# Kernel optimization log

Hardware: AMD Instinct MI355X
Metric: run time of the kernel (lower is better)

Reference implementation:

```python
import jax, jax.numpy as jnp
import numpy as np

B, L, K, D = 8, 4096, 16, 128


def setup_inputs() -> dict:
    key = jax.random.key(0)
    k1, k2 = jax.random.split(key)
    frame = jax.random.normal(k1, (B, L, 4, 3), dtype=jnp.float32)  # [B,L,4,3]: row0=center, rows1-3=frame axes
    attr = jax.random.normal(k2, (B, L, D), dtype=jnp.float32)
    return {"frame": frame, "attr": attr}


def reference(frame, attr):
    Kmax = 16
    center = frame[:, :, 0]  # [B,L,3]
    # pairwise squared distances (no grad needed through topk selection)
    c_ng = jax.lax.stop_gradient(center)
    diff = c_ng[:, :, None, :] - c_ng[:, None, :, :]  # [B,L,L,3]
    distance_sq = jnp.sum(diff * diff, axis=-1)  # [B,L,L]
    # k nearest neighbors (smallest distance)
    _, nbr = jax.lax.top_k(-distance_sq, Kmax)  # [B,L,K] int32 indices
    # gather neighbor attributes: attr[b, nbr[b,l,k], :]
    gathered_attr = jax.vmap(lambda a, i: a[i])(attr, nbr)  # [B,L,K,D]
    # gather neighbor centers and project delta into local frame
    nbr_center = jax.vmap(lambda c, i: c[i])(center, nbr)  # [B,L,K,3]
    delta = nbr_center - center[:, :, None, :]  # [B,L,K,3]
    euclidian = jnp.einsum('blkc,blcr->blkr', delta, frame[:, :, 1:4])  # [B,L,K,3]
    return (euclidian, gathered_attr)
```

## Files before the change

kernel.cpp:

```cpp
#include <hip/hip_runtime.h>
#include <stdint.h>

typedef unsigned long long u64;
typedef float nfloat4 __attribute__((ext_vector_type(4)));

#define LQ   4096
#define BQ   8
#define KNB  16
#define LPQ  8
#define TPB  256
#define QPB  (TPB / LPQ)
#define BPB  (LQ / QPB)

__device__ __forceinline__ double dmin(double a, double b) { return __builtin_fmin(a, b); }
__device__ __forceinline__ double dmax(double a, double b) { return __builtin_fmax(a, b); }


__global__ __launch_bounds__(TPB) void knn_fused_kernel(
    const float4* __restrict__ frame4,
    const float4* __restrict__ attr4,
    float* __restrict__ out_e,
    nfloat4* __restrict__ outg4)
{
    __shared__ float4 cpos[LQ];
    __shared__ int nbrs[QPB * KNB];

    const int b    = blockIdx.x >> 7;
    const int qblk = blockIdx.x & (BPB - 1);
    const int tid  = threadIdx.x;

    const float4* fb = frame4 + (size_t)b * LQ * 3;
    for (int j = tid; j < LQ; j += TPB) cpos[j] = fb[j * 3];
    __syncthreads();

    const int qloc = tid >> 3;
    const int h    = tid & 7;
    const int l    = qblk * QPB + qloc;
    const float4 me = cpos[l];

    double R[KNB];
#pragma unroll
    for (int i = 0; i < KNB; ++i) R[i] = 1.0;

#pragma unroll 1
    for (int bb = 0; bb < 32; ++bb) {
        double S[KNB];
#pragma unroll
        for (int t = 0; t < 16; ++t) {
            const int j = bb * 128 + t * 8 + h;
            const float4 p = cpos[j];
            const float dx = __fsub_rn(me.x, p.x);
            const float dy = __fsub_rn(me.y, p.y);
            const float dz = __fsub_rn(me.z, p.z);
            const float d  = __fadd_rn(__fadd_rn(__fmul_rn(dx, dx), __fmul_rn(dy, dy)),
                                       __fmul_rn(dz, dz));
            const u64 key = ((u64)__float_as_uint(d) << 12) | (unsigned)j;
            S[t] = __builtin_bit_cast(double, key);
        }
#pragma unroll
        for (int k = 2; k <= 16; k <<= 1) {
#pragma unroll
            for (int g = k >> 1; g >= 1; g >>= 1) {
#pragma unroll
                for (int i = 0; i < 16; ++i) {
                    if ((i & g) == 0) {
                        const int j2 = i + g;
                        const bool up = ((i & k) == 0);
                        const double lo = dmin(S[i], S[j2]);
                        const double hi = dmax(S[i], S[j2]);
                        S[i]  = up ? lo : hi;
                        S[j2] = up ? hi : lo;
                    }
                }
            }
        }
        double M[KNB];
#pragma unroll
        for (int i = 0; i < 16; ++i) M[i] = dmin(R[i], S[15 - i]);
#pragma unroll
        for (int g = 8; g >= 1; g >>= 1) {
#pragma unroll
            for (int i = 0; i < 16; ++i) {
                if ((i & g) == 0) {
                    const double lo = dmin(M[i], M[i + g]);
                    const double hi = dmax(M[i], M[i + g]);
                    M[i]     = lo;
                    M[i + g] = hi;
                }
            }
        }
#pragma unroll
        for (int i = 0; i < 16; ++i) R[i] = M[i];
    }

#pragma unroll
    for (int m = 1; m <= 4; m <<= 1) {
        double P[KNB];
#pragma unroll
        for (int i = 0; i < 16; ++i) P[i] = __shfl_xor(R[i], m, 64);
        double M[KNB];
#pragma unroll
        for (int i = 0; i < 16; ++i) M[i] = dmin(R[i], P[15 - i]);
#pragma unroll
        for (int g = 8; g >= 1; g >>= 1) {
#pragma unroll
            for (int i = 0; i < 16; ++i) {
                if ((i & g) == 0) {
                    const double lo = dmin(M[i], M[i + g]);
                    const double hi = dmax(M[i], M[i + g]);
                    M[i]     = lo;
                    M[i + g] = hi;
                }
            }
        }
#pragma unroll
        for (int i = 0; i < 16; ++i) R[i] = M[i];
    }

    if (h == 0) {
        const size_t gq = (size_t)b * LQ + l;
        const float4 f1 = fb[l * 3 + 1];
        const float4 f2 = fb[l * 3 + 2];
        const float R00 = me.w, R01 = f1.x, R02 = f1.y;
        const float R10 = f1.z, R11 = f1.w, R12 = f2.x;
        const float R20 = f2.y, R21 = f2.z, R22 = f2.w;

        float ebuf[48];
#pragma unroll
        for (int k = 0; k < KNB; ++k) {
            const u64 bits = __builtin_bit_cast(u64, R[k]);
            const int j = (int)(bits & 0xFFFu);
            nbrs[qloc * KNB + k] = j;
            const float4 p = cpos[j];
            const float dx = p.x - me.x;
            const float dy = p.y - me.y;
            const float dz = p.z - me.z;
            ebuf[k * 3 + 0] = dx * R00 + dy * R10 + dz * R20;
            ebuf[k * 3 + 1] = dx * R01 + dy * R11 + dz * R21;
            ebuf[k * 3 + 2] = dx * R02 + dy * R12 + dz * R22;
        }
        float4* eo = (float4*)(out_e + gq * 48);
#pragma unroll
        for (int t = 0; t < 12; ++t) eo[t] = ((const float4*)ebuf)[t];
    }

    __syncthreads();
    const float4* ab = attr4 + (((size_t)b) << 12) * 32;
    const size_t obase = ((size_t)b * LQ + (size_t)qblk * QPB) * (KNB * 32);
#pragma unroll 8
    for (int it = 0; it < 64; ++it) {
        const int fl   = it * TPB + tid;
        const int d4   = fl & 31;
        const int pair = fl >> 5;
        const int nb   = nbrs[pair];
        const float4 t4 = ab[(size_t)nb * 32 + d4];
        nfloat4 v = {t4.x, t4.y, t4.z, t4.w};
        __builtin_nontemporal_store(v, &outg4[obase + fl]);
    }
}

extern "C" void kernel_launch(void* const* d_in, const int* in_sizes, int n_in,
                              void* d_out, int out_size, void* d_ws, size_t ws_size,
                              hipStream_t stream)
{
    const float* frame = (const float*)d_in[0];
    const float* attr  = (const float*)d_in[1];
    float* out = (float*)d_out;

    nfloat4* outg4 = (nfloat4*)(out + (size_t)BQ * LQ * KNB * 3);
    knn_fused_kernel<<<BQ * BPB, TPB, 0, stream>>>(
        (const float4*)frame, (const float4*)attr, out, outg4);
}
```

Baseline: 363.5 us.

## Use truncated 32-bit keys for KNN filtering with exact double-key refinement

The candidate scan now packs a truncated distance (low 12 mantissa bits replaced by the index) into a 32-bit key. It runs an 8-element sort network plus a bitonic merge with integer compare-exchange instead of 64-bit fmin/fmax. The 32 best candidates per query are then re-ranked across lanes with exact 64-bit keys, so the final choice still matches the reference ordering. Positions move to SoA shared arrays, and the euclidean output is spread over four lanes. The attribute gather is re-indexed per wave so the block-wide barrier can be dropped. The risk is that heavy ties in the truncated keys could push a true neighbor out of the 32 survivors.

```diff
diff --git a/kernel.cpp b/kernel.cpp
--- a/kernel.cpp
+++ b/kernel.cpp
@@ -7,13 +7,28 @@
 #define LQ   4096
 #define BQ   8
 #define KNB  16
-#define LPQ  8
 #define TPB  256
-#define QPB  (TPB / LPQ)
+#define QPB  32
 #define BPB  (LQ / QPB)
 
-__device__ __forceinline__ double dmin(double a, double b) { return __builtin_fmin(a, b); }
-__device__ __forceinline__ double dmax(double a, double b) { return __builtin_fmax(a, b); }
+__device__ __forceinline__ void ceu(uint32_t &a, uint32_t &b) {
+    const uint32_t mn = a < b ? a : b;
+    const uint32_t mx = a < b ? b : a;
+    a = mn; b = mx;
+}
+__device__ __forceinline__ void ced(double &a, double &b) {
+    const double mn = __builtin_fmin(a, b);
+    const double mx = __builtin_fmax(a, b);
+    a = mn; b = mx;
+}
+__device__ __forceinline__ float dist2(float mx, float my, float mz,
+                                       float px, float py, float pz) {
+    const float dx = __fsub_rn(mx, px);
+    const float dy = __fsub_rn(my, py);
+    const float dz = __fsub_rn(mz, pz);
+    return __fadd_rn(__fadd_rn(__fmul_rn(dx, dx), __fmul_rn(dy, dy)),
+                     __fmul_rn(dz, dz));
+}
 
 
 __global__ __launch_bounds__(TPB) void knn_fused_kernel(
@@ -22,140 +37,247 @@
     float* __restrict__ out_e,
     nfloat4* __restrict__ outg4)
 {
-    __shared__ float4 cpos[LQ];
-    __shared__ int nbrs[QPB * KNB];
+    __shared__ float xs[LQ], ys[LQ], zs[LQ];
+    __shared__ unsigned short surv[QPB][32];
+    __shared__ int nbrs[QPB][KNB];
 
     const int b    = blockIdx.x >> 7;
     const int qblk = blockIdx.x & (BPB - 1);
     const int tid  = threadIdx.x;
 
     const float4* fb = frame4 + (size_t)b * LQ * 3;
-    for (int j = tid; j < LQ; j += TPB) cpos[j] = fb[j * 3];
+    for (int j = tid; j < LQ; j += TPB) {
+        const float4 v = fb[j * 3];
+        xs[j] = v.x; ys[j] = v.y; zs[j] = v.z;
+    }
     __syncthreads();
 
     const int qloc = tid >> 3;
     const int h    = tid & 7;
     const int l    = qblk * QPB + qloc;
-    const float4 me = cpos[l];
-
-    double R[KNB];
-#pragma unroll
-    for (int i = 0; i < KNB; ++i) R[i] = 1.0;
+    const float mx = xs[l], my = ys[l], mz = zs[l];
+
+    uint32_t R[16];
+#pragma unroll
+    for (int i = 0; i < 16; ++i) R[i] = 0xFFFFFFFFu;
 
 #pragma unroll 1
-    for (int bb = 0; bb < 32; ++bb) {
-        double S[KNB];
-#pragma unroll
-        for (int t = 0; t < 16; ++t) {
-            const int j = bb * 128 + t * 8 + h;
-            const float4 p = cpos[j];
-            const float dx = __fsub_rn(me.x, p.x);
-            const float dy = __fsub_rn(me.y, p.y);
-            const float dz = __fsub_rn(me.z, p.z);
-            const float d  = __fadd_rn(__fadd_rn(__fmul_rn(dx, dx), __fmul_rn(dy, dy)),
-                                       __fmul_rn(dz, dz));
-            const u64 key = ((u64)__float_as_uint(d) << 12) | (unsigned)j;
-            S[t] = __builtin_bit_cast(double, key);
-        }
-#pragma unroll
-        for (int k = 2; k <= 16; k <<= 1) {
-#pragma unroll
-            for (int g = k >> 1; g >= 1; g >>= 1) {
-#pragma unroll
-                for (int i = 0; i < 16; ++i) {
-                    if ((i & g) == 0) {
-                        const int j2 = i + g;
-                        const bool up = ((i & k) == 0);
-                        const double lo = dmin(S[i], S[j2]);
-                        const double hi = dmax(S[i], S[j2]);
-                        S[i]  = up ? lo : hi;
-                        S[j2] = up ? hi : lo;
-                    }
-                }
-            }
-        }
-        double M[KNB];
-#pragma unroll
-        for (int i = 0; i < 16; ++i) M[i] = dmin(R[i], S[15 - i]);
-#pragma unroll
-        for (int g = 8; g >= 1; g >>= 1) {
-#pragma unroll
-            for (int i = 0; i < 16; ++i) {
-                if ((i & g) == 0) {
-                    const double lo = dmin(M[i], M[i + g]);
-                    const double hi = dmax(M[i], M[i + g]);
-                    M[i]     = lo;
-                    M[i + g] = hi;
-                }
-            }
-        }
-#pragma unroll
-        for (int i = 0; i < 16; ++i) R[i] = M[i];
-    }
-
-#pragma unroll
-    for (int m = 1; m <= 4; m <<= 1) {
-        double P[KNB];
-#pragma unroll
-        for (int i = 0; i < 16; ++i) P[i] = __shfl_xor(R[i], m, 64);
-        double M[KNB];
-#pragma unroll
-        for (int i = 0; i < 16; ++i) M[i] = dmin(R[i], P[15 - i]);
-#pragma unroll
-        for (int g = 8; g >= 1; g >>= 1) {
-#pragma unroll
-            for (int i = 0; i < 16; ++i) {
-                if ((i & g) == 0) {
-                    const double lo = dmin(M[i], M[i + g]);
-                    const double hi = dmax(M[i], M[i + g]);
-                    M[i]     = lo;
-                    M[i + g] = hi;
-                }
-            }
-        }
-#pragma unroll
-        for (int i = 0; i < 16; ++i) R[i] = M[i];
-    }
-
-    if (h == 0) {
-        const size_t gq = (size_t)b * LQ + l;
+    for (int cc = 0; cc < 64; ++cc) {
+        uint32_t K[8];
+#pragma unroll
+        for (int s = 0; s < 8; ++s) {
+            const int j = cc * 64 + s * 8 + h;
+            const float d = dist2(mx, my, mz, xs[j], ys[j], zs[j]);
+            K[s] = (__float_as_uint(d) & 0xFFFFF000u) | (unsigned)j;
+        }
+        ceu(K[0],K[1]); ceu(K[2],K[3]); ceu(K[4],K[5]); ceu(K[6],K[7]);
+        ceu(K[0],K[2]); ceu(K[1],K[3]); ceu(K[4],K[6]); ceu(K[5],K[7]);
+        ceu(K[1],K[2]); ceu(K[5],K[6]);
+        ceu(K[0],K[4]); ceu(K[1],K[5]); ceu(K[2],K[6]); ceu(K[3],K[7]);
+        ceu(K[2],K[4]); ceu(K[3],K[5]);
+        ceu(K[1],K[2]); ceu(K[3],K[4]); ceu(K[5],K[6]);
+#pragma unroll
+        for (int t = 0; t < 8; ++t) {
+            const uint32_t x = R[8 + t], y = K[7 - t];
+            R[8 + t] = x < y ? x : y;
+        }
+#pragma unroll
+        for (int g = 8; g >= 1; g >>= 1)
+#pragma unroll
+            for (int i = 0; i < 16; ++i)
+                if ((i & g) == 0) ceu(R[i], R[i + g]);
+    }
+
+    {
+        uint32_t P[16];
+#pragma unroll
+        for (int i = 0; i < 16; ++i) P[i] = __shfl_xor(R[i], 1, 64);
+        const bool lo = (h & 1) == 0;
+#pragma unroll
+        for (int i = 0; i < 16; ++i) {
+            const uint32_t o = P[15 - i];
+            R[i] = lo ? (R[i] < o ? R[i] : o) : (R[i] > o ? R[i] : o);
+        }
+#pragma unroll
+        for (int g = 8; g >= 1; g >>= 1)
+#pragma unroll
+            for (int i = 0; i < 16; ++i)
+                if ((i & g) == 0) ceu(R[i], R[i + g]);
+    }
+    {
+        uint32_t P[16];
+#pragma unroll
+        for (int i = 0; i < 16; ++i) P[i] = __shfl_xor(R[i], 3, 64);
+        const bool lo = (h & 2) == 0;
+#pragma unroll
+        for (int i = 0; i < 16; ++i) {
+            const uint32_t o = P[15 - i];
+            R[i] = lo ? (R[i] < o ? R[i] : o) : (R[i] > o ? R[i] : o);
+        }
+#pragma unroll
+        for (int i = 0; i < 16; ++i) P[i] = __shfl_xor(R[i], 1, 64);
+        const bool lo1 = (h & 1) == 0;
+#pragma unroll
+        for (int i = 0; i < 16; ++i) {
+            const uint32_t o = P[i];
+            R[i] = lo1 ? (R[i] < o ? R[i] : o) : (R[i] > o ? R[i] : o);
+        }
+#pragma unroll
+        for (int g = 8; g >= 1; g >>= 1)
+#pragma unroll
+            for (int i = 0; i < 16; ++i)
+                if ((i & g) == 0) ceu(R[i], R[i + g]);
+    }
+    {
+        uint32_t P[16];
+#pragma unroll
+        for (int i = 0; i < 16; ++i) P[i] = __shfl_xor(R[i], 7, 64);
+        const bool lo = (h & 4) == 0;
+#pragma unroll
+        for (int i = 0; i < 16; ++i) {
+            const uint32_t o = P[15 - i];
+            R[i] = lo ? (R[i] < o ? R[i] : o) : (R[i] > o ? R[i] : o);
+        }
+#pragma unroll
+        for (int i = 0; i < 16; ++i) P[i] = __shfl_xor(R[i], 2, 64);
+        const bool lo2 = (h & 2) == 0;
+#pragma unroll
+        for (int i = 0; i < 16; ++i) {
+            const uint32_t o = P[i];
+            R[i] = lo2 ? (R[i] < o ? R[i] : o) : (R[i] > o ? R[i] : o);
+        }
+#pragma unroll
+        for (int i = 0; i < 16; ++i) P[i] = __shfl_xor(R[i], 1, 64);
+        const bool lo1 = (h & 1) == 0;
+#pragma unroll
+        for (int i = 0; i < 16; ++i) {
+            const uint32_t o = P[i];
+            R[i] = lo1 ? (R[i] < o ? R[i] : o) : (R[i] > o ? R[i] : o);
+        }
+#pragma unroll
+        for (int g = 8; g >= 1; g >>= 1)
+#pragma unroll
+            for (int i = 0; i < 16; ++i)
+                if ((i & g) == 0) ceu(R[i], R[i + g]);
+    }
+
+    if (h < 2) {
+#pragma unroll
+        for (int i = 0; i < 16; ++i)
+            surv[qloc][h * 16 + i] = (unsigned short)(R[i] & 0xFFFu);
+    }
+
+    double kd[4];
+#pragma unroll
+    for (int s = 0; s < 4; ++s) {
+        const int j = surv[qloc][h * 4 + s];
+        const float d = dist2(mx, my, mz, xs[j], ys[j], zs[j]);
+        kd[s] = __builtin_bit_cast(double,
+                 ((u64)__float_as_uint(d) << 12) | (unsigned)j);
+    }
+    ced(kd[0],kd[1]); ced(kd[2],kd[3]); ced(kd[0],kd[2]); ced(kd[1],kd[3]); ced(kd[1],kd[2]);
+    {
+        double P[4];
+#pragma unroll
+        for (int s = 0; s < 4; ++s) P[s] = __shfl_xor(kd[s], 1, 64);
+        const bool lo = (h & 1) == 0;
+#pragma unroll
+        for (int s = 0; s < 4; ++s) {
+            const double o = P[3 - s];
+            kd[s] = lo ? __builtin_fmin(kd[s], o) : __builtin_fmax(kd[s], o);
+        }
+        ced(kd[0],kd[2]); ced(kd[1],kd[3]); ced(kd[0],kd[1]); ced(kd[2],kd[3]);
+    }
+    {
+        double P[4];
+#pragma unroll
+        for (int s = 0; s < 4; ++s) P[s] = __shfl_xor(kd[s], 3, 64);
+        const bool lo = (h & 2) == 0;
+#pragma unroll
+        for (int s = 0; s < 4; ++s) {
+            const double o = P[3 - s];
+            kd[s] = lo ? __builtin_fmin(kd[s], o) : __builtin_fmax(kd[s], o);
+        }
+#pragma unroll
+        for (int s = 0; s < 4; ++s) P[s] = __shfl_xor(kd[s], 1, 64);
+        const bool lo1 = (h & 1) == 0;
+#pragma unroll
+        for (int s = 0; s < 4; ++s) {
+            const double o = P[s];
+            kd[s] = lo1 ? __builtin_fmin(kd[s], o) : __builtin_fmax(kd[s], o);
+        }
+        ced(kd[0],kd[2]); ced(kd[1],kd[3]); ced(kd[0],kd[1]); ced(kd[2],kd[3]);
+    }
+    {
+        double P[4];
+#pragma unroll
+        for (int s = 0; s < 4; ++s) P[s] = __shfl_xor(kd[s], 7, 64);
+        const bool lo = (h & 4) == 0;
+#pragma unroll
+        for (int s = 0; s < 4; ++s) {
+            const double o = P[3 - s];
+            kd[s] = lo ? __builtin_fmin(kd[s], o) : __builtin_fmax(kd[s], o);
+        }
+#pragma unroll
+        for (int s = 0; s < 4; ++s) P[s] = __shfl_xor(kd[s], 2, 64);
+        const bool lo2 = (h & 2) == 0;
+#pragma unroll
+        for (int s = 0; s < 4; ++s) {
+            const double o = P[s];
+            kd[s] = lo2 ? __builtin_fmin(kd[s], o) : __builtin_fmax(kd[s], o);
+        }
+#pragma unroll
+        for (int s = 0; s < 4; ++s) P[s] = __shfl_xor(kd[s], 1, 64);
+        const bool lo1 = (h & 1) == 0;
+#pragma unroll
+        for (int s = 0; s < 4; ++s) {
+            const double o = P[s];
+            kd[s] = lo1 ? __builtin_fmin(kd[s], o) : __builtin_fmax(kd[s], o);
+        }
+        ced(kd[0],kd[2]); ced(kd[1],kd[3]); ced(kd[0],kd[1]); ced(kd[2],kd[3]);
+    }
+
+    const size_t gq = (size_t)b * LQ + l;
+    if (h < 4) {
+        const float4 f0 = fb[l * 3 + 0];
         const float4 f1 = fb[l * 3 + 1];
         const float4 f2 = fb[l * 3 + 2];
-        const float R00 = me.w, R01 = f1.x, R02 = f1.y;
+        const float R00 = f0.w, R01 = f1.x, R02 = f1.y;
         const float R10 = f1.z, R11 = f1.w, R12 = f2.x;
         const float R20 = f2.y, R21 = f2.z, R22 = f2.w;
-
-        float ebuf[48];
-#pragma unroll
-        for (int k = 0; k < KNB; ++k) {
-            const u64 bits = __builtin_bit_cast(u64, R[k]);
+        float e[12];
+#pragma unroll
+        for (int s = 0; s < 4; ++s) {
+            const u64 bits = __builtin_bit_cast(u64, kd[s]);
             const int j = (int)(bits & 0xFFFu);
-            nbrs[qloc * KNB + k] = j;
-            const float4 p = cpos[j];
-            const float dx = p.x - me.x;
-            const float dy = p.y - me.y;
-            const float dz = p.z - me.z;
-            ebuf[k * 3 + 0] = dx * R00 + dy * R10 + dz * R20;
-            ebuf[k * 3 + 1] = dx * R01 + dy * R11 + dz * R21;
-            ebuf[k * 3 + 2] = dx * R02 + dy * R12 + dz * R22;
-        }
-        float4* eo = (float4*)(out_e + gq * 48);
-#pragma unroll
-        for (int t = 0; t < 12; ++t) eo[t] = ((const float4*)ebuf)[t];
-    }
-
-    __syncthreads();
+            nbrs[qloc][h * 4 + s] = j;
+            const float dx = xs[j] - mx;
+            const float dy = ys[j] - my;
+            const float dz = zs[j] - mz;
+            e[s * 3 + 0] = dx * R00 + dy * R10 + dz * R20;
+            e[s * 3 + 1] = dx * R01 + dy * R11 + dz * R21;
+            e[s * 3 + 2] = dx * R02 + dy * R12 + dz * R22;
+        }
+        float4* eo = (float4*)(out_e + gq * 48 + h * 12);
+        float4 v0 = {e[0], e[1], e[2],  e[3]};
+        float4 v1 = {e[4], e[5], e[6],  e[7]};
+        float4 v2 = {e[8], e[9], e[10], e[11]};
+        eo[0] = v0; eo[1] = v1; eo[2] = v2;
+    }
+
     const float4* ab = attr4 + (((size_t)b) << 12) * 32;
-    const size_t obase = ((size_t)b * LQ + (size_t)qblk * QPB) * (KNB * 32);
-#pragma unroll 8
+    const int wv = tid >> 6, lane = tid & 63;
+    const size_t obase = ((size_t)b * LQ + (size_t)qblk * QPB + (size_t)wv * 8) * 512;
+#pragma unroll 4
     for (int it = 0; it < 64; ++it) {
-        const int fl   = it * TPB + tid;
-        const int d4   = fl & 31;
-        const int pair = fl >> 5;
-        const int nb   = nbrs[pair];
-        const float4 t4 = ab[(size_t)nb * 32 + d4];
-        nfloat4 v = {t4.x, t4.y, t4.z, t4.w};
-        __builtin_nontemporal_store(v, &outg4[obase + fl]);
+        const int idx = it * 64 + lane;
+        const int qw  = idx >> 9;
+        const int r   = idx & 511;
+        const int k   = r >> 5, d4 = r & 31;
+        const int nb  = nbrs[wv * 8 + qw][k];
+        const float4 v = ab[(size_t)nb * 32 + d4];
+        nfloat4 nv = {v.x, v.y, v.z, v.w};
+        __builtin_nontemporal_store(nv, &outg4[obase + idx]);
     }
 }
 
```

Result: faster. 329.1 us (-9.5%).
